# Performance work log

Hardware: AMD Instinct MI355X
Metric: run time of the kernel (lower is better)

Reference implementation:

```python
import jax, jax.numpy as jnp
import numpy as np

V, E, H, B, T, S = 32000, 512, 512, 16, 128, 128


def setup_inputs() -> dict:
    key = jax.random.key(0)
    ks = jax.random.split(key, 12)
    sc_e = 1.0 / np.sqrt(E)
    sc_h = 1.0 / np.sqrt(H)
    emb_table = jax.random.normal(ks[0], (V, E), jnp.float32) * 0.02
    emb_table = emb_table.at[0].set(0.0)  # padding_idx=0
    return {
        "text_vec": jax.random.randint(ks[1], (B, T), 0, V),
        "decoder_hidden": jax.random.normal(ks[2], (1, B, H), jnp.float32),
        "encoder_output": jax.random.normal(ks[3], (B, S, H), jnp.float32),
        "attention_mask": jnp.ones((B, S), jnp.bool_),
        "emb_table": emb_table,
        "w_ih": jax.random.uniform(ks[4], (3 * H, E), jnp.float32, -sc_h, sc_h),
        "w_hh": jax.random.uniform(ks[5], (3 * H, H), jnp.float32, -sc_h, sc_h),
        "b_ih": jax.random.uniform(ks[6], (3 * H,), jnp.float32, -sc_h, sc_h),
        "b_hh": jax.random.uniform(ks[7], (3 * H,), jnp.float32, -sc_h, sc_h),
        "lin_out_w": jax.random.uniform(ks[8], (H, 2 * H), jnp.float32, -1.0 / np.sqrt(2 * H), 1.0 / np.sqrt(2 * H)),
        "out_w": jax.random.uniform(ks[9], (V, H), jnp.float32, -sc_h, sc_h),
        "out_b": jax.random.uniform(ks[10], (V,), jnp.float32, -sc_h, sc_h),
    }


def _gru_cell(x, h, w_ih, w_hh, b_ih, b_hh):
    gi = x @ w_ih.T + b_ih  # [B,3H]
    gh = h @ w_hh.T + b_hh  # [B,3H]
    ir, iz, inn = jnp.split(gi, 3, axis=-1)
    hr, hz, hn = jnp.split(gh, 3, axis=-1)
    r = jax.nn.sigmoid(ir + hr)
    z = jax.nn.sigmoid(iz + hz)
    n = jnp.tanh(inn + r * hn)
    return (1.0 - z) * n + z * h


def reference(text_vec, decoder_hidden, encoder_output, attention_mask,
              emb_table, w_ih, w_hh, b_ih, b_hh, lin_out_w, out_w, out_b):
    # embedding with padding_idx=0 -> zero vector
    emb = emb_table[text_vec] * (text_vec != 0)[..., None].astype(emb_table.dtype)  # [B,T,E]
    neg = jnp.asarray(-1e6, emb.dtype)

    def step(h, x_t):
        h_new = _gru_cell(x_t, h, w_ih, w_hh, b_ih, b_hh)  # [B,H]
        scores = jnp.einsum('bh,bsh->bs', h_new, encoder_output)
        scores = jnp.where(attention_mask, scores, neg)
        attn_w = jax.nn.softmax(scores, axis=-1)  # [B,S]
        mix = jnp.einsum('bs,bsh->bh', attn_w, encoder_output)
        combined = jnp.concatenate([h_new, mix], axis=-1)  # [B,2H]
        attended = jnp.tanh(combined @ lin_out_w.T)  # [B,H]
        return h_new, (attended, attn_w)

    h0 = decoder_hidden[0]  # num_layers == 1
    h_final, (attended_seq, attn_w_log) = jax.lax.scan(step, h0, jnp.swapaxes(emb, 0, 1))
    output = jnp.swapaxes(attended_seq, 0, 1)  # [B,T,H]
    scores = output @ out_w.T + out_b  # [B,T,V]
    return scores, h_final[None], attn_w_log
```

## Files before the change

kernel.cpp:

```cpp
#include <hip/hip_runtime.h>
#include <hip/hip_bf16.h>

#define NV 32000
#define NE 512
#define NH 512
#define NB 16
#define NT 128
#define NS 128

typedef __bf16 bf16x8 __attribute__((ext_vector_type(8)));
typedef float f32x4 __attribute__((ext_vector_type(4)));
typedef const __attribute__((address_space(1))) unsigned int gu32;
typedef __attribute__((address_space(3))) unsigned int lu32;

static constexpr size_t HTAG_OFF = 0;
static constexpr size_t WHHT_OFF = HTAG_OFF + (size_t)2*NB*NH*8;
static constexpr size_t GI_OFF   = WHHT_OFF + (size_t)3*NH*NH*4;
static constexpr size_t HALL_OFF = GI_OFF + (size_t)NT*NB*3*NH*4;
static constexpr size_t MIX_OFF  = HALL_OFF + (size_t)(NT+1)*NB*NH*4;
static constexpr size_t ATTB_OFF = MIX_OFF + (size_t)NB*NT*NH*4;
static constexpr size_t OWB_OFF  = ATTB_OFF + (size_t)NB*NT*NH*2;
static constexpr size_t WS_NEED  = OWB_OFF + (size_t)NV*NH*2;

__global__ __launch_bounds__(256) void k_pg(const int* __restrict__ tv,
                                            const float* __restrict__ emb,
                                            const float* __restrict__ w_ih,
                                            const float* __restrict__ b_ih,
                                            float* __restrict__ gi_all,
                                            const float* __restrict__ w_hh,
                                            const float* __restrict__ dh,
                                            const float* __restrict__ out_w,
                                            float* __restrict__ whhT,
                                            float* __restrict__ h_all,
                                            __bf16* __restrict__ owb,
                                            unsigned long long* __restrict__ htag) {
  const int g = blockIdx.x;
  const int tid = threadIdx.x;
  if (g >= 768) {
    long long i0 = (long long)(g - 768) * 256 + tid;
    long long stride = (long long)1024 * 256;
    long long n4 = (long long)NV * NH / 4;
    for (long long i = i0; i < n4; i += stride) {
      float4 v = ((const float4*)out_w)[i];
      union { __bf16 b[4]; float2 f2; } u;
      u.b[0] = (__bf16)v.x; u.b[1] = (__bf16)v.y; u.b[2] = (__bf16)v.z; u.b[3] = (__bf16)v.w;
      *((float2*)(owb + 4 * i)) = u.f2;
    }
    for (long long i = i0; i < (long long)3 * NH * NH; i += stride) {
      int k = (int)(i / (3 * NH)), j = (int)(i % (3 * NH));
      whhT[i] = w_hh[(long long)j * NH + k];
    }
    for (long long i = i0; i < NB * NH; i += stride) {
      float hv = dh[i];
      h_all[i] = hv;
      union { float f; unsigned u; } c; c.f = hv;
      htag[i] = (1ull << 32) | c.u;
      htag[NB * NH + i] = 0ull;
    }
    return;
  }
  __shared__ float As[16][64];
  __shared__ float Bs[16][64];
  const int n0 = (g % 24) * 64;
  const int m0 = (g / 24) * 64;
  float acc[4][4] = {};
  const int rl = tid >> 2;
  const int kq = (tid & 3) * 4;
  const int tvr = tv[m0 + rl];
  const float* arow = emb + (long long)tvr * NE;
  const int tm = tid & 15, tn = tid >> 4;
  for (int k0 = 0; k0 < NE; k0 += 16) {
    __syncthreads();
    float4 av = make_float4(0.f, 0.f, 0.f, 0.f);
    if (tvr != 0) av = *(const float4*)(arow + k0 + kq);
    float4 bv = *(const float4*)(w_ih + (long long)(n0 + rl) * NE + k0 + kq);
    As[kq + 0][rl] = av.x; As[kq + 1][rl] = av.y; As[kq + 2][rl] = av.z; As[kq + 3][rl] = av.w;
    Bs[kq + 0][rl] = bv.x; Bs[kq + 1][rl] = bv.y; Bs[kq + 2][rl] = bv.z; Bs[kq + 3][rl] = bv.w;
    __syncthreads();
#pragma unroll
    for (int kk = 0; kk < 16; ++kk) {
      float4 a = *(const float4*)&As[kk][tm * 4];
      float4 b = *(const float4*)&Bs[kk][tn * 4];
      float ar[4] = {a.x, a.y, a.z, a.w}, br[4] = {b.x, b.y, b.z, b.w};
#pragma unroll
      for (int i = 0; i < 4; ++i)
#pragma unroll
        for (int j = 0; j < 4; ++j) acc[i][j] = fmaf(ar[i], br[j], acc[i][j]);
    }
  }
#pragma unroll
  for (int i = 0; i < 4; ++i) {
    int r = m0 + tm * 4 + i;
    long long gb = (long long)((r & 127) * 16 + (r >> 7)) * (3 * NH);
#pragma unroll
    for (int j = 0; j < 4; ++j) {
      int jg = n0 + tn * 4 + j;
      gi_all[gb + jg] = acc[i][j] + b_ih[jg];
    }
  }
}

__global__ __launch_bounds__(512, 2) void k_rec(const float* __restrict__ whhT,
                                                const float* __restrict__ gi_all,
                                                const float* __restrict__ b_hh,
                                                float* __restrict__ h_all,
                                                unsigned long long* __restrict__ htag,
                                                float* __restrict__ d_hf) {
  const int tid = threadIdx.x;
  const int b = blockIdx.x & 15, sub = blockIdx.x >> 4;
  const int hl = tid & 63, kc = tid >> 6;
  const int j = sub * 64 + hl;
  __shared__ float hbuf[512];
  __shared__ float part[3][8][64];

  float wg[3][64];
#pragma unroll
  for (int g = 0; g < 3; ++g) {
    const float* wp = whhT + (long long)(kc * 64) * 1536 + g * 512 + j;
#pragma unroll
    for (int q = 0; q < 64; ++q) wg[g][q] = wp[(long long)q * 1536];
  }
  float bhr = 0.f, bhz = 0.f, bhn = 0.f;
  if (tid < 64) {
    bhr = b_hh[sub * 64 + tid];
    bhz = b_hh[512 + sub * 64 + tid];
    bhn = b_hh[1024 + sub * 64 + tid];
  }

  for (int t = 0; t < NT; ++t) {
    float gr = 0.f, gz = 0.f, gn = 0.f;
    if (tid < 64) {
      const float* gi = gi_all + (long long)(t * 16 + b) * 1536;
      gr = gi[sub * 64 + tid];
      gz = gi[512 + sub * 64 + tid];
      gn = gi[1024 + sub * 64 + tid];
    }
    {
      unsigned long long* slot = htag + ((long long)(t & 1) * NB + b) * 512 + tid;
      unsigned long long v = __hip_atomic_load(slot, __ATOMIC_RELAXED, __HIP_MEMORY_SCOPE_AGENT);
      int guard = 0;
      while ((unsigned)(v >> 32) != (unsigned)(t + 1) && ++guard < (1 << 22)) {
        v = __hip_atomic_load(slot, __ATOMIC_RELAXED, __HIP_MEMORY_SCOPE_AGENT);
      }
      union { unsigned u; float f; } c; c.u = (unsigned)v;
      hbuf[tid] = c.f;
    }
    __syncthreads();
    float ar = 0.f, az = 0.f, an = 0.f;
#pragma unroll
    for (int q4 = 0; q4 < 4; ++q4) {
      float4 h4[4];
#pragma unroll
      for (int u = 0; u < 4; ++u) h4[u] = *(const float4*)&hbuf[kc * 64 + q4 * 16 + u * 4];
#pragma unroll
      for (int u = 0; u < 4; ++u) {
        const float hh[4] = {h4[u].x, h4[u].y, h4[u].z, h4[u].w};
#pragma unroll
        for (int v = 0; v < 4; ++v) {
          const int q = q4 * 16 + u * 4 + v;
          ar = fmaf(hh[v], wg[0][q], ar);
          az = fmaf(hh[v], wg[1][q], az);
          an = fmaf(hh[v], wg[2][q], an);
        }
      }
    }
    part[0][kc][hl] = ar; part[1][kc][hl] = az; part[2][kc][hl] = an;
    __syncthreads();
    if (tid < 64) {
      float sr = bhr, sz = bhz, sn = bhn;
#pragma unroll
      for (int c = 0; c < 8; ++c) {
        sr += part[0][c][tid]; sz += part[1][c][tid]; sn += part[2][c][tid];
      }
      float r = 1.f / (1.f + expf(-(gr + sr)));
      float z = 1.f / (1.f + expf(-(gz + sz)));
      float n = tanhf(gn + r * sn);
      float hp = hbuf[sub * 64 + tid];
      float hv = (1.f - z) * n + z * hp;
      if (t < NT - 1) {
        union { float f; unsigned u; } c2; c2.f = hv;
        unsigned long long out = ((unsigned long long)(unsigned)(t + 2) << 32) | c2.u;
        __hip_atomic_store(htag + ((long long)((t + 1) & 1) * NB + b) * 512 + sub * 64 + tid, out,
                           __ATOMIC_RELAXED, __HIP_MEMORY_SCOPE_AGENT);
      }
      h_all[(long long)((t + 1) * 16 + b) * 512 + sub * 64 + tid] = hv;
      if (t == NT - 1) d_hf[b * 512 + sub * 64 + tid] = hv;
    }
    __syncthreads();
  }
}

__global__ __launch_bounds__(256) void k_attn(const float* __restrict__ h_all,
                                              const float* __restrict__ enc,
                                              const int* __restrict__ mask,
                                              float* __restrict__ d_attn,
                                              float* __restrict__ mix) {
  const int g = blockIdx.x;
  const int t = g >> 4, b = g & 15;
  const int tid = threadIdx.x;
  __shared__ float hb[512];
  __shared__ float red[256];
  __shared__ float wb[128];
  __shared__ float smax, ssum;
  const float* hsrc = h_all + (long long)((t + 1) * 16 + b) * 512;
  hb[tid] = hsrc[tid];
  hb[tid + 256] = hsrc[tid + 256];
  __syncthreads();
  const int s = tid & 127, half = tid >> 7;
  const float* erow = enc + (long long)(b * 128 + s) * 512 + half * 256;
  float p = 0.f;
#pragma unroll 8
  for (int k = 0; k < 256; ++k) p = fmaf(hb[half * 256 + k], erow[k], p);
  red[tid] = p;
  __syncthreads();
  float sc = 0.f;
  if (tid < 128) {
    sc = red[tid] + red[tid + 128];
    if (mask[b * 128 + tid] == 0) sc = -1e6f;
    wb[tid] = sc;
  }
  __syncthreads();
  if (tid < 64) {
    float m2 = fmaxf(wb[tid], wb[tid + 64]);
    for (int off = 32; off; off >>= 1) m2 = fmaxf(m2, __shfl_down(m2, off));
    if (tid == 0) smax = m2;
  }
  __syncthreads();
  if (tid < 128) wb[tid] = expf(sc - smax);
  __syncthreads();
  if (tid < 64) {
    float s2 = wb[tid] + wb[tid + 64];
    for (int off = 32; off; off >>= 1) s2 += __shfl_down(s2, off);
    if (tid == 0) ssum = s2;
  }
  __syncthreads();
  float inv = 1.f / ssum;
  if (tid < 128) {
    float w = wb[tid] * inv;
    wb[tid] = w;
    d_attn[(long long)(t * 16 + b) * 128 + tid] = w;
  }
  __syncthreads();
  long long mrow = (long long)(b * 128 + t) * 512;
  for (int hh = tid; hh < 512; hh += 256) {
    float acc = 0.f;
#pragma unroll 8
    for (int s2 = 0; s2 < 128; ++s2) acc = fmaf(wb[s2], enc[(long long)(b * 128 + s2) * 512 + hh], acc);
    mix[mrow + hh] = acc;
  }
}

__global__ __launch_bounds__(256) void k_att_lin(const float* __restrict__ h_all,
                                                 const float* __restrict__ mix,
                                                 const float* __restrict__ W,
                                                 __bf16* __restrict__ attout) {
  __shared__ float As[16][64];
  __shared__ float Bs[16][64];
  const int tid = threadIdx.x;
  const int n0 = blockIdx.x * 64;
  const int m0 = blockIdx.y * 64;
  float acc[4][4] = {};
  const int rl = tid >> 2;
  const int kq = (tid & 3) * 4;
  const int tm = tid & 15, tn = tid >> 4;
  const int r_a = m0 + rl;
  const int b_a = r_a >> 7, t_a = r_a & 127;
  const float* hrow = h_all + (long long)((t_a + 1) * 16 + b_a) * 512;
  const float* mrow = mix + (long long)r_a * 512;
  for (int k0 = 0; k0 < 1024; k0 += 16) {
    __syncthreads();
    float4 av = (k0 < 512) ? *(const float4*)(hrow + k0 + kq)
                           : *(const float4*)(mrow + (k0 - 512) + kq);
    float4 bv = *(const float4*)(W + (long long)(n0 + rl) * 1024 + k0 + kq);
    As[kq + 0][rl] = av.x; As[kq + 1][rl] = av.y; As[kq + 2][rl] = av.z; As[kq + 3][rl] = av.w;
    Bs[kq + 0][rl] = bv.x; Bs[kq + 1][rl] = bv.y; Bs[kq + 2][rl] = bv.z; Bs[kq + 3][rl] = bv.w;
    __syncthreads();
#pragma unroll
    for (int kk = 0; kk < 16; ++kk) {
      float4 a = *(const float4*)&As[kk][tm * 4];
      float4 b = *(const float4*)&Bs[kk][tn * 4];
      float ar[4] = {a.x, a.y, a.z, a.w}, br[4] = {b.x, b.y, b.z, b.w};
#pragma unroll
      for (int i = 0; i < 4; ++i)
#pragma unroll
        for (int j = 0; j < 4; ++j) acc[i][j] = fmaf(ar[i], br[j], acc[i][j]);
    }
  }
#pragma unroll
  for (int i = 0; i < 4; ++i) {
    int r = m0 + tm * 4 + i;
#pragma unroll
    for (int j = 0; j < 4; ++j) {
      int o = n0 + tn * 4 + j;
      attout[(long long)r * 512 + o] = (__bf16)tanhf(acc[i][j]);
    }
  }
}

__global__ __launch_bounds__(256) void k_out(const __bf16* __restrict__ Abf,
                                             const __bf16* __restrict__ Bbf,
                                             const float* __restrict__ bias,
                                             float* __restrict__ Cout) {
  __shared__ __bf16 Al[128 * 32];
  __shared__ __bf16 Bl[128 * 32];
  const int tid = threadIdx.x;
  const int lane = tid & 63;
  const int wave = tid >> 6;
  const int wm = wave >> 1, wn = wave & 1;
  const int swz = (blockIdx.x & 7) * 500 + (blockIdx.x >> 3);
  const int m0 = (swz & 15) * 128, n0 = (swz >> 4) * 128;
  f32x4 acc[4][4] = {};
  const int lrow = lane >> 2;
  const int lcol = (lane & 3) * 8;
  const int lm = lane & 15, lc = lane >> 4;
  for (int ks = 0; ks < 16; ++ks) {
    const int k0 = ks * 32;
    __syncthreads();
#pragma unroll
    for (int i = 0; i < 2; ++i) {
      int chunk = wave * 2 + i;
      int r = chunk * 16 + lrow;
      const __bf16* ga = Abf + (long long)(m0 + r) * NH + k0 + lcol;
      const __bf16* gb = Bbf + (long long)(n0 + r) * NH + k0 + lcol;
      __builtin_amdgcn_global_load_lds((gu32*)ga, (lu32*)((char*)Al + chunk * 1024), 16, 0, 0);
      __builtin_amdgcn_global_load_lds((gu32*)gb, (lu32*)((char*)Bl + chunk * 1024), 16, 0, 0);
    }
    __syncthreads();
    bf16x8 af[4], bfr[4];
#pragma unroll
    for (int i = 0; i < 4; ++i) af[i] = *(const bf16x8*)&Al[(wm * 64 + i * 16 + lm) * 32 + lc * 8];
#pragma unroll
    for (int j = 0; j < 4; ++j) bfr[j] = *(const bf16x8*)&Bl[(wn * 64 + j * 16 + lm) * 32 + lc * 8];
#pragma unroll
    for (int i = 0; i < 4; ++i)
#pragma unroll
      for (int j = 0; j < 4; ++j)
        acc[i][j] = __builtin_amdgcn_mfma_f32_16x16x32_bf16(bfr[j], af[i], acc[i][j], 0, 0, 0);
  }
  float4 bv[4];
#pragma unroll
  for (int j = 0; j < 4; ++j)
    bv[j] = *(const float4*)&bias[n0 + wn * 64 + j * 16 + lc * 4];
#pragma unroll
  for (int i = 0; i < 4; ++i) {
    long long rbase = (long long)(m0 + wm * 64 + i * 16 + lm) * NV;
#pragma unroll
    for (int j = 0; j < 4; ++j) {
      int c = n0 + wn * 64 + j * 16 + lc * 4;
      float4 o;
      o.x = acc[i][j][0] + bv[j].x;
      o.y = acc[i][j][1] + bv[j].y;
      o.z = acc[i][j][2] + bv[j].z;
      o.w = acc[i][j][3] + bv[j].w;
      *(float4*)&Cout[rbase + c] = o;
    }
  }
}

extern "C" void kernel_launch(void* const* d_in, const int* in_sizes, int n_in,
                              void* d_out, int out_size, void* d_ws, size_t ws_size,
                              hipStream_t stream) {
  const int* tv = (const int*)d_in[0];
  const float* dh = (const float*)d_in[1];
  const float* enc = (const float*)d_in[2];
  const int* mask = (const int*)d_in[3];
  const float* emb = (const float*)d_in[4];
  const float* w_ih = (const float*)d_in[5];
  const float* w_hh = (const float*)d_in[6];
  const float* b_ih = (const float*)d_in[7];
  const float* b_hh = (const float*)d_in[8];
  const float* lin_w = (const float*)d_in[9];
  const float* out_w = (const float*)d_in[10];
  const float* out_b = (const float*)d_in[11];
  float* dout = (float*)d_out;
  char* ws = (char*)d_ws;
  if (ws_size < WS_NEED) return;

  unsigned long long* htag = (unsigned long long*)(ws + HTAG_OFF);
  float* whhT = (float*)(ws + WHHT_OFF);
  float* gi_all = (float*)(ws + GI_OFF);
  float* h_all = (float*)(ws + HALL_OFF);
  float* mixb = (float*)(ws + MIX_OFF);
  __bf16* attb = (__bf16*)(ws + ATTB_OFF);
  __bf16* owb = (__bf16*)(ws + OWB_OFF);

  float* d_scores = dout;
  float* d_hf = dout + (long long)NB * NT * NV;
  float* d_attn = d_hf + NB * NH;

  k_pg<<<1792, 256, 0, stream>>>(tv, emb, w_ih, b_ih, gi_all,
                                 w_hh, dh, out_w, whhT, h_all, owb, htag);
  k_rec<<<128, 512, 0, stream>>>(whhT, gi_all, b_hh, h_all, htag, d_hf);
  k_attn<<<2048, 256, 0, stream>>>(h_all, enc, mask, d_attn, mixb);
  k_att_lin<<<dim3(8, 32), 256, 0, stream>>>(h_all, mixb, lin_w, attb);
  k_out<<<4000, 256, 0, stream>>>(attb, owb, out_b, d_scores);
}
```

Measured before the change: 578.3 us.

## Fuse GRU recurrence with attention and weight conversion in a persistent kernel

The recurrence and attention kernels are merged into one 256-block persistent launch. 128 blocks run the GRU with 1024 threads each, which splits the K dimension 16 ways. The other 128 blocks first convert out_w to bf16 and then compute attention for each timestep as soon as a per-(t,b) done counter reports that step's hidden state is ready. This overlaps the latency-bound serial recurrence with the attention and conversion work instead of running them back to back. The cost is cross-block spin-waiting, which relies on all 256 blocks being co-resident, and an 86KB shared allocation that may reduce occupancy.

After: 725.4 us. 1.25x slower.

```diff
diff --git a/kernel.cpp b/kernel.cpp
--- a/kernel.cpp
+++ b/kernel.cpp
@@ -13,14 +13,15 @@
 typedef const __attribute__((address_space(1))) unsigned int gu32;
 typedef __attribute__((address_space(3))) unsigned int lu32;
 
-static constexpr size_t HTAG_OFF = 0;
-static constexpr size_t WHHT_OFF = HTAG_OFF + (size_t)2*NB*NH*8;
-static constexpr size_t GI_OFF   = WHHT_OFF + (size_t)3*NH*NH*4;
-static constexpr size_t HALL_OFF = GI_OFF + (size_t)NT*NB*3*NH*4;
-static constexpr size_t MIX_OFF  = HALL_OFF + (size_t)(NT+1)*NB*NH*4;
-static constexpr size_t ATTB_OFF = MIX_OFF + (size_t)NB*NT*NH*4;
-static constexpr size_t OWB_OFF  = ATTB_OFF + (size_t)NB*NT*NH*2;
-static constexpr size_t WS_NEED  = OWB_OFF + (size_t)NV*NH*2;
+static constexpr size_t HTAG_OFF  = 0;
+static constexpr size_t HDONE_OFF = HTAG_OFF + (size_t)2*NB*NH*8;
+static constexpr size_t WHHT_OFF  = HDONE_OFF + 8192;
+static constexpr size_t GI_OFF    = WHHT_OFF + (size_t)3*NH*NH*4;
+static constexpr size_t HALL_OFF  = GI_OFF + (size_t)NT*NB*3*NH*4;
+static constexpr size_t MIX_OFF   = HALL_OFF + (size_t)(NT+1)*NB*NH*4;
+static constexpr size_t ATTB_OFF  = MIX_OFF + (size_t)NB*NT*NH*4;
+static constexpr size_t OWB_OFF   = ATTB_OFF + (size_t)NB*NT*NH*2;
+static constexpr size_t WS_NEED   = OWB_OFF + (size_t)NV*NH*2;
 
 __global__ __launch_bounds__(256) void k_pg(const int* __restrict__ tv,
                                             const float* __restrict__ emb,
@@ -29,23 +30,15 @@
                                             float* __restrict__ gi_all,
                                             const float* __restrict__ w_hh,
                                             const float* __restrict__ dh,
-                                            const float* __restrict__ out_w,
                                             float* __restrict__ whhT,
                                             float* __restrict__ h_all,
-                                            __bf16* __restrict__ owb,
-                                            unsigned long long* __restrict__ htag) {
+                                            unsigned long long* __restrict__ htag,
+                                            unsigned int* __restrict__ hdone) {
   const int g = blockIdx.x;
   const int tid = threadIdx.x;
   if (g >= 768) {
     long long i0 = (long long)(g - 768) * 256 + tid;
-    long long stride = (long long)1024 * 256;
-    long long n4 = (long long)NV * NH / 4;
-    for (long long i = i0; i < n4; i += stride) {
-      float4 v = ((const float4*)out_w)[i];
-      union { __bf16 b[4]; float2 f2; } u;
-      u.b[0] = (__bf16)v.x; u.b[1] = (__bf16)v.y; u.b[2] = (__bf16)v.z; u.b[3] = (__bf16)v.w;
-      *((float2*)(owb + 4 * i)) = u.f2;
-    }
+    long long stride = (long long)256 * 256;
     for (long long i = i0; i < (long long)3 * NH * NH; i += stride) {
       int k = (int)(i / (3 * NH)), j = (int)(i % (3 * NH));
       whhT[i] = w_hh[(long long)j * NH + k];
@@ -57,6 +50,7 @@
       htag[i] = (1ull << 32) | c.u;
       htag[NB * NH + i] = 0ull;
     }
+    for (long long i = i0; i < 2048; i += stride) hdone[i] = 0u;
     return;
   }
   __shared__ float As[16][64];
@@ -100,153 +94,188 @@
   }
 }
 
-__global__ __launch_bounds__(512, 2) void k_rec(const float* __restrict__ whhT,
-                                                const float* __restrict__ gi_all,
-                                                const float* __restrict__ b_hh,
-                                                float* __restrict__ h_all,
-                                                unsigned long long* __restrict__ htag,
-                                                float* __restrict__ d_hf) {
+__global__ __launch_bounds__(1024) void k_mid(const float* __restrict__ whhT,
+                                              const float* __restrict__ gi_all,
+                                              const float* __restrict__ b_hh,
+                                              float* __restrict__ h_all,
+                                              unsigned long long* __restrict__ htag,
+                                              unsigned int* __restrict__ hdone,
+                                              float* __restrict__ d_hf,
+                                              const float* __restrict__ enc,
+                                              const int* __restrict__ mask,
+                                              const float* __restrict__ out_w,
+                                              __bf16* __restrict__ owb,
+                                              float* __restrict__ d_attn,
+                                              float* __restrict__ mixb) {
+  __shared__ char smem_raw[86016];
+  float* smem = (float*)smem_raw;
   const int tid = threadIdx.x;
-  const int b = blockIdx.x & 15, sub = blockIdx.x >> 4;
-  const int hl = tid & 63, kc = tid >> 6;
-  const int j = sub * 64 + hl;
-  __shared__ float hbuf[512];
-  __shared__ float part[3][8][64];
-
-  float wg[3][64];
-#pragma unroll
-  for (int g = 0; g < 3; ++g) {
-    const float* wp = whhT + (long long)(kc * 64) * 1536 + g * 512 + j;
-#pragma unroll
-    for (int q = 0; q < 64; ++q) wg[g][q] = wp[(long long)q * 1536];
-  }
-  float bhr = 0.f, bhz = 0.f, bhn = 0.f;
-  if (tid < 64) {
-    bhr = b_hh[sub * 64 + tid];
-    bhz = b_hh[512 + sub * 64 + tid];
-    bhn = b_hh[1024 + sub * 64 + tid];
-  }
-
-  for (int t = 0; t < NT; ++t) {
-    float gr = 0.f, gz = 0.f, gn = 0.f;
+  const int bid = blockIdx.x;
+
+  if (bid < 128) {
+    const int b = bid & 15, sub = bid >> 4;
+    const int hl = tid & 63, kc = tid >> 6;
+    const int j = sub * 64 + hl;
+    float* hbuf = smem;
+    float* part = smem + 512;
+
+    float wg[3][32];
+#pragma unroll
+    for (int g = 0; g < 3; ++g) {
+      const float* wp = whhT + (long long)(kc * 32) * 1536 + g * 512 + j;
+#pragma unroll
+      for (int q = 0; q < 32; ++q) wg[g][q] = wp[(long long)q * 1536];
+    }
+    float bhr = 0.f, bhz = 0.f, bhn = 0.f;
     if (tid < 64) {
-      const float* gi = gi_all + (long long)(t * 16 + b) * 1536;
-      gr = gi[sub * 64 + tid];
-      gz = gi[512 + sub * 64 + tid];
-      gn = gi[1024 + sub * 64 + tid];
-    }
-    {
-      unsigned long long* slot = htag + ((long long)(t & 1) * NB + b) * 512 + tid;
-      unsigned long long v = __hip_atomic_load(slot, __ATOMIC_RELAXED, __HIP_MEMORY_SCOPE_AGENT);
-      int guard = 0;
-      while ((unsigned)(v >> 32) != (unsigned)(t + 1) && ++guard < (1 << 22)) {
-        v = __hip_atomic_load(slot, __ATOMIC_RELAXED, __HIP_MEMORY_SCOPE_AGENT);
-      }
-      union { unsigned u; float f; } c; c.u = (unsigned)v;
-      hbuf[tid] = c.f;
-    }
-    __syncthreads();
-    float ar = 0.f, az = 0.f, an = 0.f;
-#pragma unroll
-    for (int q4 = 0; q4 < 4; ++q4) {
-      float4 h4[4];
-#pragma unroll
-      for (int u = 0; u < 4; ++u) h4[u] = *(const float4*)&hbuf[kc * 64 + q4 * 16 + u * 4];
-#pragma unroll
-      for (int u = 0; u < 4; ++u) {
-        const float hh[4] = {h4[u].x, h4[u].y, h4[u].z, h4[u].w};
+      bhr = b_hh[sub * 64 + tid];
+      bhz = b_hh[512 + sub * 64 + tid];
+      bhn = b_hh[1024 + sub * 64 + tid];
+    }
+
+    for (int t = 0; t < NT; ++t) {
+      float gr = 0.f, gz = 0.f, gn = 0.f;
+      if (tid < 64) {
+        const float* gi = gi_all + (long long)(t * 16 + b) * 1536;
+        gr = gi[sub * 64 + tid];
+        gz = gi[512 + sub * 64 + tid];
+        gn = gi[1024 + sub * 64 + tid];
+      }
+      if (tid < 512) {
+        unsigned long long* slot = htag + ((long long)(t & 1) * NB + b) * 512 + tid;
+        unsigned long long v = __hip_atomic_load(slot, __ATOMIC_RELAXED, __HIP_MEMORY_SCOPE_AGENT);
+        int guard = 0;
+        while ((unsigned)(v >> 32) != (unsigned)(t + 1) && ++guard < (1 << 22)) {
+          v = __hip_atomic_load(slot, __ATOMIC_RELAXED, __HIP_MEMORY_SCOPE_AGENT);
+        }
+        union { unsigned u; float f; } c; c.u = (unsigned)v;
+        hbuf[tid] = c.f;
+      }
+      __syncthreads();
+      float ar = 0.f, az = 0.f, an = 0.f;
+#pragma unroll
+      for (int q4 = 0; q4 < 8; ++q4) {
+        float4 h4 = *(const float4*)&hbuf[kc * 32 + q4 * 4];
+        const float hh[4] = {h4.x, h4.y, h4.z, h4.w};
 #pragma unroll
         for (int v = 0; v < 4; ++v) {
-          const int q = q4 * 16 + u * 4 + v;
+          const int q = q4 * 4 + v;
           ar = fmaf(hh[v], wg[0][q], ar);
           az = fmaf(hh[v], wg[1][q], az);
           an = fmaf(hh[v], wg[2][q], an);
         }
       }
-    }
-    part[0][kc][hl] = ar; part[1][kc][hl] = az; part[2][kc][hl] = an;
+      part[(0 * 16 + kc) * 64 + hl] = ar;
+      part[(1 * 16 + kc) * 64 + hl] = az;
+      part[(2 * 16 + kc) * 64 + hl] = an;
+      __syncthreads();
+      if (tid < 64) {
+        float sr = bhr, sz = bhz, sn = bhn;
+#pragma unroll
+        for (int c = 0; c < 16; ++c) {
+          sr += part[(0 * 16 + c) * 64 + tid];
+          sz += part[(1 * 16 + c) * 64 + tid];
+          sn += part[(2 * 16 + c) * 64 + tid];
+        }
+        float r = 1.f / (1.f + expf(-(gr + sr)));
+        float z = 1.f / (1.f + expf(-(gz + sz)));
+        float n = tanhf(gn + r * sn);
+        float hp = hbuf[sub * 64 + tid];
+        float hv = (1.f - z) * n + z * hp;
+        if (t < NT - 1) {
+          union { float f; unsigned u; } c2; c2.f = hv;
+          unsigned long long out = ((unsigned long long)(unsigned)(t + 2) << 32) | c2.u;
+          __hip_atomic_store(htag + ((long long)((t + 1) & 1) * NB + b) * 512 + sub * 64 + tid, out,
+                             __ATOMIC_RELAXED, __HIP_MEMORY_SCOPE_AGENT);
+        }
+        __hip_atomic_store(&h_all[(long long)((t + 1) * 16 + b) * 512 + sub * 64 + tid], hv,
+                           __ATOMIC_RELAXED, __HIP_MEMORY_SCOPE_AGENT);
+        if (t == NT - 1) d_hf[b * 512 + sub * 64 + tid] = hv;
+      }
+      __syncthreads();
+      if (tid == 0)
+        __hip_atomic_fetch_add(&hdone[t * 16 + b], 1u, __ATOMIC_RELAXED, __HIP_MEMORY_SCOPE_AGENT);
+    }
+    return;
+  }
+
+  const int cid = bid - 128;
+  {
+    long long n4 = (long long)NV * NH / 4;
+    for (long long i = (long long)cid * 1024 + tid; i < n4; i += (long long)128 * 1024) {
+      float4 v = ((const float4*)out_w)[i];
+      union { __bf16 b[4]; float2 f2; } u;
+      u.b[0] = (__bf16)v.x; u.b[1] = (__bf16)v.y; u.b[2] = (__bf16)v.z; u.b[3] = (__bf16)v.w;
+      *((float2*)((__bf16*)owb + 4 * i)) = u.f2;
+    }
+  }
+  float* hb = smem;
+  float* red = smem + 512;
+  float* wb = smem + 1536;
+  float* sred = smem + 1664;
+  for (int it = 0; it < 16; ++it) {
+    const int u = it * 128 + cid;
+    const int t = u >> 4, b = u & 15;
+    if (tid == 0) {
+      int guard = 0;
+      while (__hip_atomic_load(&hdone[u], __ATOMIC_RELAXED, __HIP_MEMORY_SCOPE_AGENT) < 8u &&
+             ++guard < (1 << 25)) {
+        __builtin_amdgcn_s_sleep(4);
+      }
+    }
+    __syncthreads();
+    if (tid < 512)
+      hb[tid] = __hip_atomic_load(&h_all[(long long)((t + 1) * 16 + b) * 512 + tid],
+                                  __ATOMIC_RELAXED, __HIP_MEMORY_SCOPE_AGENT);
+    __syncthreads();
+    {
+      const int s = tid & 127, q8 = tid >> 7;
+      const float* erow = enc + (long long)(b * 128 + s) * 512 + q8 * 64;
+      float p = 0.f;
+#pragma unroll 8
+      for (int k = 0; k < 64; ++k) p = fmaf(hb[q8 * 64 + k], erow[k], p);
+      red[tid] = p;
+    }
+    __syncthreads();
+    float sc = 0.f;
+    if (tid < 128) {
+#pragma unroll
+      for (int c = 0; c < 8; ++c) sc += red[c * 128 + tid];
+      if (mask[b * 128 + tid] == 0) sc = -1e6f;
+      wb[tid] = sc;
+    }
     __syncthreads();
     if (tid < 64) {
-      float sr = bhr, sz = bhz, sn = bhn;
-#pragma unroll
-      for (int c = 0; c < 8; ++c) {
-        sr += part[0][c][tid]; sz += part[1][c][tid]; sn += part[2][c][tid];
-      }
-      float r = 1.f / (1.f + expf(-(gr + sr)));
-      float z = 1.f / (1.f + expf(-(gz + sz)));
-      float n = tanhf(gn + r * sn);
-      float hp = hbuf[sub * 64 + tid];
-      float hv = (1.f - z) * n + z * hp;
-      if (t < NT - 1) {
-        union { float f; unsigned u; } c2; c2.f = hv;
-        unsigned long long out = ((unsigned long long)(unsigned)(t + 2) << 32) | c2.u;
-        __hip_atomic_store(htag + ((long long)((t + 1) & 1) * NB + b) * 512 + sub * 64 + tid, out,
-                           __ATOMIC_RELAXED, __HIP_MEMORY_SCOPE_AGENT);
-      }
-      h_all[(long long)((t + 1) * 16 + b) * 512 + sub * 64 + tid] = hv;
-      if (t == NT - 1) d_hf[b * 512 + sub * 64 + tid] = hv;
-    }
-    __syncthreads();
-  }
-}
-
-__global__ __launch_bounds__(256) void k_attn(const float* __restrict__ h_all,
-                                              const float* __restrict__ enc,
-                                              const int* __restrict__ mask,
-                                              float* __restrict__ d_attn,
-                                              float* __restrict__ mix) {
-  const int g = blockIdx.x;
-  const int t = g >> 4, b = g & 15;
-  const int tid = threadIdx.x;
-  __shared__ float hb[512];
-  __shared__ float red[256];
-  __shared__ float wb[128];
-  __shared__ float smax, ssum;
-  const float* hsrc = h_all + (long long)((t + 1) * 16 + b) * 512;
-  hb[tid] = hsrc[tid];
-  hb[tid + 256] = hsrc[tid + 256];
-  __syncthreads();
-  const int s = tid & 127, half = tid >> 7;
-  const float* erow = enc + (long long)(b * 128 + s) * 512 + half * 256;
-  float p = 0.f;
+      float m2 = fmaxf(wb[tid], wb[tid + 64]);
+      for (int off = 32; off; off >>= 1) m2 = fmaxf(m2, __shfl_down(m2, off));
+      if (tid == 0) sred[0] = m2;
+    }
+    __syncthreads();
+    if (tid < 128) wb[tid] = expf(sc - sred[0]);
+    __syncthreads();
+    if (tid < 64) {
+      float s2 = wb[tid] + wb[tid + 64];
+      for (int off = 32; off; off >>= 1) s2 += __shfl_down(s2, off);
+      if (tid == 0) sred[1] = s2;
+    }
+    __syncthreads();
+    {
+      float inv = 1.f / sred[1];
+      if (tid < 128) {
+        float w = wb[tid] * inv;
+        wb[tid] = w;
+        d_attn[(long long)u * 128 + tid] = w;
+      }
+    }
+    __syncthreads();
+    if (tid < 512) {
+      float m = 0.f;
 #pragma unroll 8
-  for (int k = 0; k < 256; ++k) p = fmaf(hb[half * 256 + k], erow[k], p);
-  red[tid] = p;
-  __syncthreads();
-  float sc = 0.f;
-  if (tid < 128) {
-    sc = red[tid] + red[tid + 128];
-    if (mask[b * 128 + tid] == 0) sc = -1e6f;
-    wb[tid] = sc;
-  }
-  __syncthreads();
-  if (tid < 64) {
-    float m2 = fmaxf(wb[tid], wb[tid + 64]);
-    for (int off = 32; off; off >>= 1) m2 = fmaxf(m2, __shfl_down(m2, off));
-    if (tid == 0) smax = m2;
-  }
-  __syncthreads();
-  if (tid < 128) wb[tid] = expf(sc - smax);
-  __syncthreads();
-  if (tid < 64) {
-    float s2 = wb[tid] + wb[tid + 64];
-    for (int off = 32; off; off >>= 1) s2 += __shfl_down(s2, off);
-    if (tid == 0) ssum = s2;
-  }
-  __syncthreads();
-  float inv = 1.f / ssum;
-  if (tid < 128) {
-    float w = wb[tid] * inv;
-    wb[tid] = w;
-    d_attn[(long long)(t * 16 + b) * 128 + tid] = w;
-  }
-  __syncthreads();
-  long long mrow = (long long)(b * 128 + t) * 512;
-  for (int hh = tid; hh < 512; hh += 256) {
-    float acc = 0.f;
-#pragma unroll 8
-    for (int s2 = 0; s2 < 128; ++s2) acc = fmaf(wb[s2], enc[(long long)(b * 128 + s2) * 512 + hh], acc);
-    mix[mrow + hh] = acc;
+      for (int s2 = 0; s2 < 128; ++s2)
+        m = fmaf(wb[s2], enc[(long long)(b * 128 + s2) * 512 + tid], m);
+      mixb[(long long)(b * 128 + t) * 512 + tid] = m;
+    }
+    __syncthreads();
   }
 }
 
@@ -377,6 +406,7 @@
   if (ws_size < WS_NEED) return;
 
   unsigned long long* htag = (unsigned long long*)(ws + HTAG_OFF);
+  unsigned int* hdone = (unsigned int*)(ws + HDONE_OFF);
   float* whhT = (float*)(ws + WHHT_OFF);
   float* gi_all = (float*)(ws + GI_OFF);
   float* h_all = (float*)(ws + HALL_OFF);
@@ -388,10 +418,10 @@
   float* d_hf = dout + (long long)NB * NT * NV;
   float* d_attn = d_hf + NB * NH;
 
-  k_pg<<<1792, 256, 0, stream>>>(tv, emb, w_ih, b_ih, gi_all,
-                                 w_hh, dh, out_w, whhT, h_all, owb, htag);
-  k_rec<<<128, 512, 0, stream>>>(whhT, gi_all, b_hh, h_all, htag, d_hf);
-  k_attn<<<2048, 256, 0, stream>>>(h_all, enc, mask, d_attn, mixb);
+  k_pg<<<1024, 256, 0, stream>>>(tv, emb, w_ih, b_ih, gi_all,
+                                 w_hh, dh, whhT, h_all, htag, hdone);
+  k_mid<<<256, 1024, 0, stream>>>(whhT, gi_all, b_hh, h_all, htag, hdone, d_hf,
+                                  enc, mask, out_w, owb, d_attn, mixb);
   k_att_lin<<<dim3(8, 32), 256, 0, stream>>>(h_all, mixb, lin_w, attb);
   k_out<<<4000, 256, 0, stream>>>(attb, owb, out_b, d_scores);
 }
```
